# Kernel optimization log

Hardware: AMD Instinct MI355X
Metric: run time of the kernel (lower is better)

Reference implementation:

```python
import jax, jax.numpy as jnp
import numpy as np

TAU = 0.001
TEMPERATURE = 0.1


def setup_inputs() -> dict:
    key = jax.random.key(0)
    k1, k2 = jax.random.split(key)
    B, H, N, L = 2, 8, 256, 64
    X = jax.random.normal(k1, (B, H, N, L), dtype=jnp.float32)
    Y = jax.random.normal(k2, (B, H, N, L), dtype=jnp.float32)
    return {"X": X, "Y": Y}


def _softsort_p2(scores):
    # scores: [B,H,N,L] -> s: [B,H,L,N]
    s = jnp.transpose(scores, (0, 1, 3, 2))
    srt = -jnp.sort(-s, axis=-1)  # descending sort along N
    # pairwise squared diff: rows = sorted values, cols = original values -> [B,H,L,N,N]
    pd = -((s[..., None, :] - srt[..., :, None]) ** 2) / TAU
    return jax.nn.softmax(pd, axis=-1)


def reference(X, Y):
    # Soft permutation matrices: [B,H,L,N,N]
    Pu = _softsort_p2(X)
    Pv = _softsort_p2(Y)
    # Gamma = Pu^T @ Pv  (contract over sorted-row index i)
    Gamma = jnp.einsum('bhlij,bhlik->bhljk', Pu, Pv)
    # cdist(X, Y, p=2) over last dim L -> [B,H,N,N]
    x2 = jnp.sum(X * X, axis=-1)            # [B,H,N]
    y2 = jnp.sum(Y * Y, axis=-1)            # [B,H,N]
    xy = jnp.einsum('bhnl,bhml->bhnm', X, Y)
    cost = jnp.sqrt(jnp.maximum(x2[..., :, None] + y2[..., None, :] - 2.0 * xy, 1e-12))
    # swds[b,h,l] = sum_{j,k} cost[b,h,j,k] * Gamma[b,h,l,j,k]
    swds = jnp.einsum('bhjk,bhljk->bhl', cost, Gamma)
    # exp(-T*(swds - min)) / sum == softmax(-T * swds) over L
    weights = jax.nn.softmax(-TEMPERATURE * swds, axis=-1)  # [B,H,L]
    # weighted sum over L -> [B,H,N,N]
    return jnp.einsum('bhljk,bhl->bhjk', Gamma, weights)
```

## Files before the change

### kernel.cpp

```cpp
#include <hip/hip_runtime.h>
#include <math.h>

#define INV_TAU 1000.0f
#define TEMP    0.1f
#define CEXP    -1442.6950408889634f
#define SQRTC   37.98283767f


typedef __attribute__((ext_vector_type(8))) _Float16 half8;
typedef __attribute__((ext_vector_type(8))) short short8;
typedef __attribute__((ext_vector_type(4))) float f32x4;
typedef __attribute__((ext_vector_type(2))) float f32x2;
typedef __attribute__((ext_vector_type(4))) unsigned int u32x4;

__device__ __forceinline__ float fexp2(float x) { return __builtin_amdgcn_exp2f(x); }

__device__ __forceinline__ half8 ldsh8(const unsigned short* p) {
  return __builtin_bit_cast(half8, *(const short8*)p);
}

__device__ __forceinline__ unsigned cvt_pk_bf16(float lo, float hi) {
  unsigned r;
  asm("v_cvt_pk_bf16_f32 %0, %1, %2" : "=v"(r) : "v"(lo), "v"(hi));
  return r;
}

__device__ __forceinline__ int tswz(int row, int g) {
  return row * 32 + (((g + (row >> 1)) & 3) << 3);
}

__global__ __launch_bounds__(256) void prep_kernel(const float* __restrict__ X,
                                                   const float* __restrict__ Y,
                                                   float* __restrict__ cost,
                                                   float* __restrict__ nssu, float* __restrict__ lziu,
                                                   float* __restrict__ nssv, float* __restrict__ lziv) {
  __shared__ __align__(16) float smem[256];
  const int tid = threadIdx.x;
  if (blockIdx.x < 1024) {
    const int jq = blockIdx.x & 63, bh = blockIdx.x >> 6;
    const int j0 = jq * 4;
    smem[tid] = X[((size_t)bh*256 + j0 + (tid >> 6))*64 + (tid & 63)];
    __syncthreads();
    const float4* yp = (const float4*)(Y + ((size_t)bh*256 + tid)*64);
    float dot[4] = {0.f,0.f,0.f,0.f}, x2[4] = {0.f,0.f,0.f,0.f}, y2 = 0.f;
#pragma unroll
    for (int t = 0; t < 16; ++t) {
      float4 yv = yp[t];
      y2 += yv.x*yv.x + yv.y*yv.y + yv.z*yv.z + yv.w*yv.w;
#pragma unroll
      for (int r = 0; r < 4; ++r) {
        float4 xv = ((const float4*)(smem + r*64))[t];
        dot[r] += xv.x*yv.x + xv.y*yv.y + xv.z*yv.z + xv.w*yv.w;
        x2[r]  += xv.x*xv.x + xv.y*xv.y + xv.z*xv.z + xv.w*xv.w;
      }
    }
#pragma unroll
    for (int r = 0; r < 4; ++r) {
      float c = x2[r] + y2 - 2.f*dot[r];
      cost[((size_t)bh*256 + j0 + r)*256 + tid] = sqrtf(fmaxf(c, 1e-12f));
    }
  } else {
    const int idx = blockIdx.x - 1024;
    const int l = idx & 63, bh = (idx >> 6) & 15, uv = idx >> 10;
    const float* S = uv ? Y : X;
    float* so = uv ? nssv : nssu;
    float* zo = uv ? lziv : lziu;
    float v = S[((size_t)bh*256 + tid)*64 + l];
#pragma unroll
    for (int k = 2; k <= 256; k <<= 1) {
#pragma unroll
      for (int j = k >> 1; j > 0; j >>= 1) {
        float o;
        if (j >= 64) {
          smem[tid] = v; __syncthreads();
          o = smem[tid ^ j]; __syncthreads();
        } else {
          o = __shfl_xor(v, j, 64);
        }
        const bool up    = ((tid & k) == 0);
        const bool lower = ((tid & j) == 0);
        float mn = fminf(v, o), mx = fmaxf(v, o);
        v = (up == lower) ? mn : mx;
      }
    }
    smem[tid] = v; __syncthreads();
    const int jc = 255 - tid;
    const float sv = smem[jc];
    int lo = jc > 48 ? jc - 48 : 0;
    const int hi = jc < 207 ? jc + 48 : 255;
    lo &= ~1;
    f32x2 z2 = {0.f, 0.f};
    const f32x2 svv = {sv, sv};
    const f32x2 cxx = {CEXP, CEXP};
    for (int p = lo; p <= hi; p += 2) {
      f32x2 s2 = *(const f32x2*)(smem + p);
      f32x2 d  = s2 - svv;
      f32x2 a  = (d * d) * cxx;
      z2 += (f32x2){fexp2(a.x), fexp2(a.y)};
    }
    const float z = z2.x + z2.y;
    const int base = (bh*64 + l)*256 + tid;
    so[base] = -SQRTC * sv; zo[base] = -__log2f(z);
  }
}

__device__ __forceinline__ u32x4 oct_exp(const float* __restrict__ nss,
                                         const float* __restrict__ lz, float sc) {
  const f32x2 sc2 = {sc, sc};
  f32x2 d0 = sc2 + *(const f32x2*)(nss + 0);
  f32x2 d1 = sc2 + *(const f32x2*)(nss + 2);
  f32x2 d2 = sc2 + *(const f32x2*)(nss + 4);
  f32x2 d3 = sc2 + *(const f32x2*)(nss + 6);
  f32x2 a0 = __builtin_elementwise_fma(-d0, d0, *(const f32x2*)(lz + 0));
  f32x2 a1 = __builtin_elementwise_fma(-d1, d1, *(const f32x2*)(lz + 2));
  f32x2 a2 = __builtin_elementwise_fma(-d2, d2, *(const f32x2*)(lz + 4));
  f32x2 a3 = __builtin_elementwise_fma(-d3, d3, *(const f32x2*)(lz + 6));
  u32x4 w;
  w[0] = __builtin_bit_cast(unsigned, __builtin_amdgcn_cvt_pkrtz(fexp2(a0.x), fexp2(a0.y)));
  w[1] = __builtin_bit_cast(unsigned, __builtin_amdgcn_cvt_pkrtz(fexp2(a1.x), fexp2(a1.y)));
  w[2] = __builtin_bit_cast(unsigned, __builtin_amdgcn_cvt_pkrtz(fexp2(a2.x), fexp2(a2.y)));
  w[3] = __builtin_bit_cast(unsigned, __builtin_amdgcn_cvt_pkrtz(fexp2(a3.x), fexp2(a3.y)));
  return w;
}

__device__ __forceinline__ void stage_slab(int t, int ib, float usc, float vsc,
                                           const float* __restrict__ nssU, const float* __restrict__ lzU,
                                           const float* __restrict__ nssV, const float* __restrict__ lzV,
                                           unsigned short* __restrict__ EU,
                                           unsigned short* __restrict__ EV) {
  {
    const int r = t & 127, g = t >> 7;
    const int i0 = ib + (g << 3);
    *(u32x4*)&EU[tswz(r, g)] = oct_exp(nssU + i0, lzU + i0, usc);
  }
  {
    const int r = t & 255;
    const int gp = (t >> 8) << 1;
#pragma unroll
    for (int gg = 0; gg < 2; ++gg) {
      const int i0 = ib + ((gp + gg) << 3);
      *(u32x4*)&EV[tswz(r, gp + gg)] = oct_exp(nssV + i0, lzV + i0, vsc);
    }
  }
}

__global__ __launch_bounds__(512, 4) void pass1_kernel(
    const float* __restrict__ X, const float* __restrict__ Y,
    const float* __restrict__ cost,
    const float* __restrict__ nssu, const float* __restrict__ lziu,
    const float* __restrict__ nssv, const float* __restrict__ lziv,
    float* __restrict__ parts, u32x4* __restrict__ gamma) {
  const int sb = blockIdx.x, l = blockIdx.y, bh = blockIdx.z;
  const int j0 = sb * 128;
  const int tid = threadIdx.x, wave = tid >> 6, lane = tid & 63;
  const int wj = (wave & 1) * 64, wk = (wave >> 1) * 64;
  const int m = lane & 15, q = lane >> 4;
  const int inner = m*32 + (((q + (m >> 1)) & 3) << 3);

  __shared__ __align__(16) float nssU[256], lzU[256], nssV[256], lzV[256];
  __shared__ __align__(16) unsigned short EU0[128*32], EU1[128*32];
  __shared__ __align__(16) unsigned short EV0[256*32], EV1[256*32];
  __shared__ float red[8];

  const int lb = (bh*64 + l)*256;
  const float usc = SQRTC * X[((size_t)bh*256 + j0 + (tid & 127))*64 + l];
  const float vsc = SQRTC * Y[((size_t)bh*256 + (tid & 255))*64 + l];
  if (tid < 256) { nssU[tid] = nssu[lb + tid]; lzU[tid] = lziu[lb + tid]; }
  else { const int t2 = tid - 256; nssV[t2] = nssv[lb + t2]; lzV[t2] = lziv[lb + t2]; }

  f32x4 acc[16];
#pragma unroll
  for (int t = 0; t < 16; ++t) acc[t] = (f32x4){0.f, 0.f, 0.f, 0.f};

  __syncthreads();
  stage_slab(tid, 0, usc, vsc, nssU, lzU, nssV, lzV, EU0, EV0);
  __syncthreads();
#pragma unroll 1
  for (int s = 0; s < 8; ++s) {
    const unsigned short* EUc = (s & 1) ? EU1 : EU0;
    const unsigned short* EVc = (s & 1) ? EV1 : EV0;
    unsigned short* EUn = (s & 1) ? EU0 : EU1;
    unsigned short* EVn = (s & 1) ? EV0 : EV1;
    half8 A[4], B[4];
#pragma unroll
    for (int mt = 0; mt < 4; ++mt) A[mt] = ldsh8(&EUc[(wj + mt*16)*32 + inner]);
#pragma unroll
    for (int nt = 0; nt < 4; ++nt) B[nt] = ldsh8(&EVc[(wk + nt*16)*32 + inner]);
    if (s < 7)
      stage_slab(tid, (s+1)*32, usc, vsc, nssU, lzU, nssV, lzV, EUn, EVn);
#pragma unroll
    for (int mt = 0; mt < 4; ++mt)
#pragma unroll
      for (int nt = 0; nt < 4; ++nt)
        acc[mt*4+nt] = __builtin_amdgcn_mfma_f32_16x16x32_f16(A[mt], B[nt], acc[mt*4+nt], 0, 0, 0);
    __syncthreads();
  }

  const float* cb = cost + (size_t)bh * 65536;
  const int c8 = ((bh*2 + sb)*8 + wave) * 8;
  float part = 0.f;
#pragma unroll
  for (int mt = 0; mt < 4; ++mt) {
#pragma unroll
    for (int nt2 = 0; nt2 < 2; ++nt2) {
      const int colA = wk + nt2*32 + m;
      const int rowb = j0 + wj + mt*16 + q*4;
      f32x4 a0 = acc[mt*4 + 2*nt2];
      f32x4 a1 = acc[mt*4 + 2*nt2 + 1];
      const float* cr0 = cb + (size_t)rowb*256;
      part += a0.x*cr0[colA]        + a0.y*cr0[256 + colA]
            + a0.z*cr0[512 + colA]  + a0.w*cr0[768 + colA]
            + a1.x*cr0[colA + 16]   + a1.y*cr0[256 + colA + 16]
            + a1.z*cr0[512 + colA + 16] + a1.w*cr0[768 + colA + 16];
      u32x4 pk;
      pk[0] = cvt_pk_bf16(a0.x, a0.y);
      pk[1] = cvt_pk_bf16(a0.z, a0.w);
      pk[2] = cvt_pk_bf16(a1.x, a1.y);
      pk[3] = cvt_pk_bf16(a1.z, a1.w);
      __builtin_nontemporal_store(pk, &gamma[((size_t)(c8 + mt*2 + nt2)*64 + l)*64 + lane]);
    }
  }
#pragma unroll
  for (int o = 32; o > 0; o >>= 1) part += __shfl_down(part, o, 64);
  if (lane == 0) red[wave] = part;
  __syncthreads();
  if (tid == 0) {
    float s8 = red[0]+red[1]+red[2]+red[3]+red[4]+red[5]+red[6]+red[7];
    parts[sb*1024 + bh*64 + l] = s8;
  }
}

__global__ __launch_bounds__(256) void wsum_kernel(const u32x4* __restrict__ g,
                                                   const float* __restrict__ parts,
                                                   float* __restrict__ out) {
  const int wv = threadIdx.x >> 6, lane = threadIdx.x & 63;
  const int c  = blockIdx.x * 4 + wv;
  const int bh = c >> 7;
  __shared__ float w[64];
  if (threadIdx.x < 64) {
    float s = parts[bh*64 + lane] + parts[1024 + bh*64 + lane];
    float v = -TEMP * s * 1.4426950408889634f;
    float mx = v;
#pragma unroll
    for (int o = 32; o > 0; o >>= 1) mx = fmaxf(mx, __shfl_xor(mx, o, 64));
    float e = fexp2(v - mx);
    float ssum = e;
#pragma unroll
    for (int o = 32; o > 0; o >>= 1) ssum += __shfl_xor(ssum, o, 64);
    w[lane] = e / ssum;
  }
  __syncthreads();
  const u32x4* gp = g + (size_t)c*4096 + lane;
  const int st = c & 63;
  float4 accA = {0.f, 0.f, 0.f, 0.f};
  float4 accB = {0.f, 0.f, 0.f, 0.f};
#pragma unroll 16
  for (int p = 0; p < 64; ++p) {
    const int l = (p + st) & 63;
    u32x4 pk = __builtin_nontemporal_load(gp + l*64);
    float wl = w[l];
    accA.x += wl * __uint_as_float(pk[0] << 16);
    accA.y += wl * __uint_as_float(pk[0] & 0xFFFF0000u);
    accA.z += wl * __uint_as_float(pk[1] << 16);
    accA.w += wl * __uint_as_float(pk[1] & 0xFFFF0000u);
    accB.x += wl * __uint_as_float(pk[2] << 16);
    accB.y += wl * __uint_as_float(pk[2] & 0xFFFF0000u);
    accB.z += wl * __uint_as_float(pk[3] << 16);
    accB.w += wl * __uint_as_float(pk[3] & 0xFFFF0000u);
  }
  const int nt2 = c & 1, mt = (c >> 1) & 3, rest = c >> 3;
  const int wave = rest & 7, sbb = (rest >> 3) & 1;
  const int m = lane & 15, q = lane >> 4;
  const int row  = sbb*128 + (wave & 1)*64 + mt*16 + q*4;
  const int colA = (wave >> 1)*64 + nt2*32 + m;
  float* ob = out + ((size_t)bh*256 + row)*256 + colA;
  __builtin_nontemporal_store(accA.x, &ob[0]);
  __builtin_nontemporal_store(accA.y, &ob[256]);
  __builtin_nontemporal_store(accA.z, &ob[512]);
  __builtin_nontemporal_store(accA.w, &ob[768]);
  __builtin_nontemporal_store(accB.x, &ob[16]);
  __builtin_nontemporal_store(accB.y, &ob[272]);
  __builtin_nontemporal_store(accB.z, &ob[528]);
  __builtin_nontemporal_store(accB.w, &ob[784]);
}

extern "C" void kernel_launch(void* const* d_in, const int* in_sizes, int n_in,
                              void* d_out, int out_size, void* d_ws, size_t ws_size,
                              hipStream_t stream) {
  (void)in_sizes; (void)n_in; (void)out_size; (void)ws_size;
  const float* X = (const float*)d_in[0];
  const float* Y = (const float*)d_in[1];
  float* out = (float*)d_out;
  float* ws  = (float*)d_ws;
  float* cost  = ws;
  float* nssu  = ws   + 1048576;
  float* lziu  = nssu + 262144;
  float* nssv  = lziu + 262144;
  float* lziv  = nssv + 262144;
  float* parts = lziv + 262144;
  u32x4* gamma = (u32x4*)(parts + 2048);

  prep_kernel <<<dim3(3072),      256, 0, stream>>>(X, Y, cost, nssu, lziu, nssv, lziv);
  pass1_kernel<<<dim3(2, 64, 16), 512, 0, stream>>>(X, Y, cost, nssu, lziu, nssv, lziv,
                                                    parts, gamma);
  wsum_kernel <<<dim3(512),       256, 0, stream>>>(gamma, parts, out);
}
```

Before: 166.1 us.

## Sort V rows by value with index tracking and skip out-of-band exp tiles

The prep sort now carries each element's original index alongside an order-preserving integer key, and the V-side log-normalizer has its low mantissa bits overwritten with that original index. Pass1 then assigns each V row by sorted rank, so each wave's 64 rows are contiguous in sorted order, and zero-fills exp octets far outside that band instead of computing exp2. This cuts the transcendental work in the staging step. It relies on the softmax being negligible beyond about 56 ranks and slightly corrupts lz values through the packed index bits. It also raises wave priority around the MFMA block.

```diff
diff --git a/kernel.cpp b/kernel.cpp
--- a/kernel.cpp
+++ b/kernel.cpp
@@ -34,7 +34,7 @@
                                                    float* __restrict__ cost,
                                                    float* __restrict__ nssu, float* __restrict__ lziu,
                                                    float* __restrict__ nssv, float* __restrict__ lziv) {
-  __shared__ __align__(16) float smem[256];
+  __shared__ __align__(16) float smem[512];
   const int tid = threadIdx.x;
   if (blockIdx.x < 1024) {
     const int jq = blockIdx.x & 63, bh = blockIdx.x >> 6;
@@ -60,37 +60,47 @@
       cost[((size_t)bh*256 + j0 + r)*256 + tid] = sqrtf(fmaxf(c, 1e-12f));
     }
   } else {
-    const int idx = blockIdx.x - 1024;
-    const int l = idx & 63, bh = (idx >> 6) & 15, uv = idx >> 10;
+    const int bidx = blockIdx.x - 1024;
+    const int l = bidx & 63, bh = (bidx >> 6) & 15, uv = bidx >> 10;
     const float* S = uv ? Y : X;
     float* so = uv ? nssv : nssu;
     float* zo = uv ? lziv : lziu;
-    float v = S[((size_t)bh*256 + tid)*64 + l];
-#pragma unroll
-    for (int k = 2; k <= 256; k <<= 1) {
-#pragma unroll
-      for (int j = k >> 1; j > 0; j >>= 1) {
-        float o;
+    const float v = S[((size_t)bh*256 + tid)*64 + l];
+    unsigned u = __float_as_uint(v);
+    unsigned k = ((int)u < 0) ? ~u : (u | 0x80000000u);
+    unsigned id = (unsigned)tid;
+#pragma unroll
+    for (int kk = 2; kk <= 256; kk <<= 1) {
+#pragma unroll
+      for (int j = kk >> 1; j > 0; j >>= 1) {
+        unsigned ok, oi;
         if (j >= 64) {
-          smem[tid] = v; __syncthreads();
-          o = smem[tid ^ j]; __syncthreads();
+          smem[tid] = __uint_as_float(k);
+          smem[256 + tid] = __uint_as_float(id);
+          __syncthreads();
+          ok = __float_as_uint(smem[tid ^ j]);
+          oi = __float_as_uint(smem[256 + (tid ^ j)]);
+          __syncthreads();
         } else {
-          o = __shfl_xor(v, j, 64);
+          ok = (unsigned)__shfl_xor((int)k, j, 64);
+          oi = (unsigned)__shfl_xor((int)id, j, 64);
         }
-        const bool up    = ((tid & k) == 0);
-        const bool lower = ((tid & j) == 0);
-        float mn = fminf(v, o), mx = fmaxf(v, o);
-        v = (up == lower) ? mn : mx;
+        const bool keepmin = ((tid & kk) == 0) == ((tid & j) == 0);
+        const bool iless = (k < ok) | ((k == ok) & (id < oi));
+        const bool take_other = keepmin ? (!iless) : iless;
+        k  = take_other ? ok : k;
+        id = take_other ? oi : id;
       }
     }
-    smem[tid] = v; __syncthreads();
-    const int jc = 255 - tid;
-    const float sv = smem[jc];
-    int lo = jc > 48 ? jc - 48 : 0;
-    const int hi = jc < 207 ? jc + 48 : 255;
+    const unsigned su = (k & 0x80000000u) ? (k ^ 0x80000000u) : ~k;
+    const float sval = __uint_as_float(su);
+    smem[tid] = sval;
+    __syncthreads();
+    int lo = tid > 48 ? tid - 48 : 0;
+    const int hi = tid < 207 ? tid + 48 : 255;
     lo &= ~1;
     f32x2 z2 = {0.f, 0.f};
-    const f32x2 svv = {sv, sv};
+    const f32x2 svv = {sval, sval};
     const f32x2 cxx = {CEXP, CEXP};
     for (int p = lo; p <= hi; p += 2) {
       f32x2 s2 = *(const f32x2*)(smem + p);
@@ -99,8 +109,16 @@
       z2 += (f32x2){fexp2(a.x), fexp2(a.y)};
     }
     const float z = z2.x + z2.y;
-    const int base = (bh*64 + l)*256 + tid;
-    so[base] = -SQRTC * sv; zo[base] = -__log2f(z);
+    const int rank = 255 - tid;
+    const int base = (bh*64 + l)*256 + rank;
+    so[base] = -SQRTC * sval;
+    const float lzv = -__log2f(z);
+    if (uv) {
+      unsigned b = (__float_as_uint(lzv) & 0xFFFFFF00u) | id;
+      zo[base] = __uint_as_float(b);
+    } else {
+      zo[base] = lzv;
+    }
   }
 }
 
@@ -123,7 +141,8 @@
   return w;
 }
 
-__device__ __forceinline__ void stage_slab(int t, int ib, float usc, float vsc,
+__device__ __forceinline__ void stage_slab(int t, int ib, float usc,
+                                           float vscR, int vrow, int rmin,
                                            const float* __restrict__ nssU, const float* __restrict__ lzU,
                                            const float* __restrict__ nssV, const float* __restrict__ lzV,
                                            unsigned short* __restrict__ EU,
@@ -134,12 +153,17 @@
     *(u32x4*)&EU[tswz(r, g)] = oct_exp(nssU + i0, lzU + i0, usc);
   }
   {
-    const int r = t & 255;
     const int gp = (t >> 8) << 1;
 #pragma unroll
     for (int gg = 0; gg < 2; ++gg) {
-      const int i0 = ib + ((gp + gg) << 3);
-      *(u32x4*)&EV[tswz(r, gp + gg)] = oct_exp(nssV + i0, lzV + i0, vsc);
+      const int g = gp + gg;
+      const int i0 = ib + (g << 3);
+      const int off = tswz(vrow, g);
+      if (i0 + 7 < rmin - 56 || i0 > rmin + 63 + 56) {
+        *(u32x4*)&EV[off] = (u32x4){0u, 0u, 0u, 0u};
+      } else {
+        *(u32x4*)&EV[off] = oct_exp(nssV + i0, lzV + i0, vscR);
+      }
     }
   }
 }
@@ -164,7 +188,6 @@
 
   const int lb = (bh*64 + l)*256;
   const float usc = SQRTC * X[((size_t)bh*256 + j0 + (tid & 127))*64 + l];
-  const float vsc = SQRTC * Y[((size_t)bh*256 + (tid & 255))*64 + l];
   if (tid < 256) { nssU[tid] = nssu[lb + tid]; lzU[tid] = lziu[lb + tid]; }
   else { const int t2 = tid - 256; nssV[t2] = nssv[lb + t2]; lzV[t2] = lziv[lb + t2]; }
 
@@ -173,7 +196,12 @@
   for (int t = 0; t < 16; ++t) acc[t] = (f32x4){0.f, 0.f, 0.f, 0.f};
 
   __syncthreads();
-  stage_slab(tid, 0, usc, vsc, nssU, lzU, nssV, lzV, EU0, EV0);
+  const int rt = tid & 255;
+  const float vscR = -nssV[rt];
+  const int vrow = (int)(__float_as_uint(lzV[rt]) & 0xFFu);
+  const int rmin = ((tid >> 6) & 3) * 64;
+
+  stage_slab(tid, 0, usc, vscR, vrow, rmin, nssU, lzU, nssV, lzV, EU0, EV0);
   __syncthreads();
 #pragma unroll 1
   for (int s = 0; s < 8; ++s) {
@@ -187,12 +215,14 @@
 #pragma unroll
     for (int nt = 0; nt < 4; ++nt) B[nt] = ldsh8(&EVc[(wk + nt*16)*32 + inner]);
     if (s < 7)
-      stage_slab(tid, (s+1)*32, usc, vsc, nssU, lzU, nssV, lzV, EUn, EVn);
+      stage_slab(tid, (s+1)*32, usc, vscR, vrow, rmin, nssU, lzU, nssV, lzV, EUn, EVn);
+    __builtin_amdgcn_s_setprio(1);
 #pragma unroll
     for (int mt = 0; mt < 4; ++mt)
 #pragma unroll
       for (int nt = 0; nt < 4; ++nt)
         acc[mt*4+nt] = __builtin_amdgcn_mfma_f32_16x16x32_f16(A[mt], B[nt], acc[mt*4+nt], 0, 0, 0);
+    __builtin_amdgcn_s_setprio(0);
     __syncthreads();
   }
 
```

New measurement: 178.3 us. 1.07x slower.
